# Kernel tuning notes

Measured on AMD Instinct MI355X. Metric: run time of the kernel, lower is better.

The kernel has to match this reference:

```python
import jax, jax.numpy as jnp
import numpy as np

NUM_TERMS = 8
NUM_CHANNELS = 64
BATCH = 8
NODES = 2048


def setup_inputs() -> dict:
    key = jax.random.key(0)
    kA, kh = jax.random.split(key)
    A = jax.random.normal(kA, (BATCH, NODES, NODES), dtype=jnp.float32)
    # xavier_uniform over (num_terms+1, num_channels)
    fan_in, fan_out = NUM_TERMS + 1, NUM_CHANNELS
    limit = float(np.sqrt(6.0 / (fan_in + fan_out)))
    h = jax.random.uniform(kh, (NUM_TERMS + 1, NUM_CHANNELS), dtype=jnp.float32,
                           minval=-limit, maxval=limit)
    return {"A": A, "h": h}


def reference(A, h):
    # Y[b,n,c] = h[0,c] + sum_{i=1..T} h[i,c] * diag(A^i)[b,n]
    num_terms = h.shape[0] - 1
    diags = []  # each [B, N]: diagonal of A^i
    Ap = A
    for i in range(num_terms):
        if i > 0:
            Ap = jnp.matmul(Ap, A)  # A^(i+1), computed once per power
        diags.append(jnp.diagonal(Ap, axis1=-2, axis2=-1))
    D = jnp.stack(diags, axis=0)  # [T, B, N]
    # fuse per-channel weighted sum of diagonals into one einsum
    out = jnp.einsum("tbn,tc->bnc", D, h[1:])
    out = out + h[0][None, None, :]  # identity term: diag(I) == 1
    return out
```

## Files before the change

kernel.cpp:

```cpp
#include <hip/hip_runtime.h>
#include <hip/hip_bf16.h>

#define NN 2048
#define BB 8
#define NC 64

typedef __bf16 bf16_8 __attribute__((ext_vector_type(8)));
typedef __bf16 bf16_4 __attribute__((ext_vector_type(4)));
typedef float f32x16 __attribute__((ext_vector_type(16)));

__device__ __forceinline__ void gll16(const void* g, void* l) {
  __builtin_amdgcn_global_load_lds((const __attribute__((address_space(1))) void*)g,
                                   (__attribute__((address_space(3))) void*)l,
                                   16, 0, 0);
}

__global__ __launch_bounds__(256)
void k_convert(const float* __restrict__ A, __bf16* __restrict__ Ab, __bf16* __restrict__ At) {
  __shared__ __bf16 tile[64][65];
  int b = blockIdx.z;
  const float* Asrc = A + (size_t)b * NN * NN;
  __bf16* Abd = Ab + (size_t)b * NN * NN;
  __bf16* Atd = At + (size_t)b * NN * NN;
  int r0 = blockIdx.y * 64, c0 = blockIdx.x * 64;
  int row = threadIdx.x >> 4;
  int col4 = (threadIdx.x & 15) * 4;
#pragma unroll
  for (int rr = 0; rr < 64; rr += 16) {
    float4 v = *(const float4*)&Asrc[(size_t)(r0 + row + rr) * NN + c0 + col4];
    bf16_4 hv;
    hv[0] = (__bf16)v.x; hv[1] = (__bf16)v.y; hv[2] = (__bf16)v.z; hv[3] = (__bf16)v.w;
    *(bf16_4*)&Abd[(size_t)(r0 + row + rr) * NN + c0 + col4] = hv;
    tile[row + rr][col4 + 0] = hv[0];
    tile[row + rr][col4 + 1] = hv[1];
    tile[row + rr][col4 + 2] = hv[2];
    tile[row + rr][col4 + 3] = hv[3];
  }
  __syncthreads();
  int row2 = threadIdx.x >> 3;
  int col8 = (threadIdx.x & 7) * 8;
#pragma unroll
  for (int rr = 0; rr < 64; rr += 32) {
    bf16_8 v;
#pragma unroll
    for (int j = 0; j < 8; ++j) v[j] = tile[col8 + j][row2 + rr];
    *(bf16_8*)&Atd[(size_t)(c0 + row2 + rr) * NN + r0 + col8] = v;
  }
}

__device__ __forceinline__
void gemm_body(const __bf16* __restrict__ Pb, const __bf16* __restrict__ Qb,
               __bf16* __restrict__ Cb, __bf16* __restrict__ Ctb,
               __bf16* smem, int tmBlk, int tnBlk) {
  __bf16 (*As)[64] = (__bf16(*)[64])smem;
  __bf16 (*Bs)[64] = (__bf16(*)[64])(smem + 16384);
  int tid = threadIdx.x;
  int wave = tid >> 6;
  int lane = tid & 63;
  int tm = tmBlk * 256;
  int tn = tnBlk * 128;
  int wm = (wave >> 1) * 128;
  int wn = (wave & 1) * 64;

  int srow = lane >> 3;
  int sc = (lane & 7) ^ srow;
  int arowA = wave * 64;
  int arowB = wave * 32;
  const __bf16* pA = Pb + (size_t)(tm + arowA + srow) * NN + sc * 8;
  const __bf16* pB = Qb + (size_t)(tn + arowB + srow) * NN + sc * 8;

  int am = lane & 31;
  int ah = lane >> 5;

  f32x16 acc[4][2] = {};

  for (int k0 = 0; k0 < NN; k0 += 64) {
#pragma unroll
    for (int g = 0; g < 8; ++g)
      gll16(pA + (size_t)(g * 8) * NN + k0, &As[arowA + g * 8][0]);
#pragma unroll
    for (int g = 0; g < 4; ++g)
      gll16(pB + (size_t)(g * 8) * NN + k0, &Bs[arowB + g * 8][0]);
    __syncthreads();
#pragma unroll
    for (int ks = 0; ks < 4; ++ks) {
      int cch = ks * 2 + ah;
      bf16_8 af[4], bf2[2];
#pragma unroll
      for (int i = 0; i < 4; ++i) {
        int ra = wm + i * 32 + am;
        af[i] = *(const bf16_8*)&As[ra][(cch ^ (ra & 7)) * 8];
      }
#pragma unroll
      for (int i = 0; i < 2; ++i) {
        int rb2 = wn + i * 32 + am;
        bf2[i] = *(const bf16_8*)&Bs[rb2][(cch ^ (rb2 & 7)) * 8];
      }
#pragma unroll
      for (int im = 0; im < 4; ++im)
#pragma unroll
        for (int in = 0; in < 2; ++in)
          acc[im][in] = __builtin_amdgcn_mfma_f32_32x32x16_bf16(af[im], bf2[in], acc[im][in], 0, 0, 0);
    }
    __syncthreads();
  }

  int cc = lane & 31;
  int rq = (lane >> 5) * 4;
#pragma unroll
  for (int im = 0; im < 4; ++im)
#pragma unroll
    for (int in = 0; in < 2; ++in)
#pragma unroll
      for (int reg = 0; reg < 16; ++reg) {
        int row = (reg & 3) + 8 * (reg >> 2) + rq;
        Cb[(size_t)(tm + wm + im * 32 + row) * NN + (tn + wn + in * 32 + cc)] =
            (__bf16)acc[im][in][reg];
      }

  if (Ctb != nullptr) {
    __bf16 (*Tt)[258] = (__bf16(*)[258])smem;
#pragma unroll
    for (int ch = 0; ch < 2; ++ch) {
      __syncthreads();
      if ((wave & 1) == ch) {
#pragma unroll
        for (int im = 0; im < 4; ++im)
#pragma unroll
          for (int in = 0; in < 2; ++in)
#pragma unroll
            for (int g = 0; g < 4; ++g) {
              bf16_4 v;
#pragma unroll
              for (int r = 0; r < 4; ++r) v[r] = (__bf16)acc[im][in][g * 4 + r];
              *(bf16_4*)&Tt[in * 32 + cc][wm + im * 32 + rq + 8 * g] = v;
            }
      }
      __syncthreads();
#pragma unroll
      for (int p = 0; p < 4; ++p) {
        int trow = p * 16 + (tid >> 4);
        int tcol = (tid & 15) * 16;
        bf16_8 v0 = *(const bf16_8*)&Tt[trow][tcol];
        bf16_8 v1 = *(const bf16_8*)&Tt[trow][tcol + 8];
        size_t gr = (size_t)(tn + ch * 64 + trow) * NN + tm + tcol;
        *(bf16_8*)&Ctb[gr] = v0;
        *(bf16_8*)&Ctb[gr + 8] = v1;
      }
    }
  }
}

__global__ __launch_bounds__(256, 2)
void k_gemm1(const __bf16* __restrict__ Ab, const __bf16* __restrict__ At,
             __bf16* __restrict__ A2, __bf16* __restrict__ A2t) {
  __shared__ __align__(16) __bf16 smem[24576];
  size_t mb = (size_t)blockIdx.z * NN * NN;
  gemm_body(Ab + mb, At + mb, A2 + mb, A2t + mb, smem, blockIdx.y, blockIdx.x);
}

__global__ __launch_bounds__(256, 3)
void k_gemm23(const __bf16* __restrict__ At, const __bf16* __restrict__ A2,
              const __bf16* __restrict__ A2t,
              __bf16* __restrict__ A3t, __bf16* __restrict__ A4,
              __bf16* __restrict__ A4t) {
  __shared__ __align__(16) __bf16 smem[24576];
  int job = blockIdx.z >> 3;
  size_t mb = (size_t)(blockIdx.z & 7) * NN * NN;
  if (job == 0)
    gemm_body(At + mb, A2 + mb, A3t + mb, nullptr, smem, blockIdx.y, blockIdx.x);
  else
    gemm_body(A2 + mb, A2t + mb, A4 + mb, A4t + mb, smem, blockIdx.y, blockIdx.x);
}

__global__ __launch_bounds__(256)
void k_reduce(const float* __restrict__ A, const float* __restrict__ h,
              const __bf16* __restrict__ A2, const __bf16* __restrict__ A3t,
              const __bf16* __restrict__ A4, const __bf16* __restrict__ A4t,
              float* __restrict__ out) {
  int b = blockIdx.y;
  int wave = threadIdx.x >> 6, lane = threadIdx.x & 63;
  int n = blockIdx.x * 4 + wave;
  size_t mb = (size_t)b * NN * NN;
  size_t rb = mb + (size_t)n * NN;
  float d5 = 0, d6 = 0, d7 = 0, d8 = 0;
  for (int c = 0; c < NN; c += 512) {
    int k = c + lane * 8;
    bf16_8 va2  = *(const bf16_8*)(A2 + rb + k);
    bf16_8 va3t = *(const bf16_8*)(A3t + rb + k);
    bf16_8 va4  = *(const bf16_8*)(A4 + rb + k);
    bf16_8 va4t = *(const bf16_8*)(A4t + rb + k);
#pragma unroll
    for (int j = 0; j < 8; ++j) {
      float f2 = (float)va2[j], f4 = (float)va4[j];
      float f3t = (float)va3t[j], f4t = (float)va4t[j];
      d5 += f2 * f3t;
      d6 += f2 * f4t;
      d7 += f4 * f3t;
      d8 += f4 * f4t;
    }
  }
#pragma unroll
  for (int off = 32; off > 0; off >>= 1) {
    d5 += __shfl_xor(d5, off);
    d6 += __shfl_xor(d6, off);
    d7 += __shfl_xor(d7, off);
    d8 += __shfl_xor(d8, off);
  }
  float d1 = A[mb + (size_t)n * NN + n];
  float d2 = (float)A2[rb + n];
  float d3 = (float)A3t[rb + n];
  float d4 = (float)A4[rb + n];
  float r = h[lane] + h[64 + lane] * d1 + h[128 + lane] * d2 + h[192 + lane] * d3 +
            h[256 + lane] * d4 + h[320 + lane] * d5 + h[384 + lane] * d6 +
            h[448 + lane] * d7 + h[512 + lane] * d8;
  out[((size_t)b * NN + n) * NC + lane] = r;
}

extern "C" void kernel_launch(void* const* d_in, const int* in_sizes, int n_in,
                              void* d_out, int out_size, void* d_ws, size_t ws_size,
                              hipStream_t stream) {
  const float* A = (const float*)d_in[0];
  const float* h = (const float*)d_in[1];
  float* out = (float*)d_out;

  size_t elems = (size_t)BB * NN * NN;
  __bf16* Ab  = (__bf16*)d_ws;
  __bf16* At  = Ab + elems;
  __bf16* A2  = At + elems;
  __bf16* A2t = A2 + elems;
  __bf16* A3t = A2t + elems;
  __bf16* A4  = A3t + elems;
  __bf16* A4t = Ab;

  dim3 bl(256);
  k_convert<<<dim3(32, 32, BB), bl, 0, stream>>>(A, Ab, At);
  k_gemm1<<<dim3(16, 8, BB), bl, 0, stream>>>(Ab, At, A2, A2t);
  k_gemm23<<<dim3(16, 8, 2 * BB), bl, 0, stream>>>(At, A2, A2t, A3t, A4, A4t);
  k_reduce<<<dim3(NN / 4, BB), bl, 0, stream>>>(A, h, A2, A3t, A4, A4t, out);
}
```

Before: 691.3 us.

## Rewrite GEMM as 256x256 tile, 8-wave kernel with double-buffered async LDS pipeline

Replaces the 256x128 tile GEMM, which had a single LDS buffer and barriers around every k-step, with a 256x256 tile on 512 threads (8 waves). A and B k-tiles are double-buffered in 128 KB of LDS. Global-to-LDS loads for later tiles are spread across eight phases and interleaved with MFMA work, using explicit vmcnt/lgkmcnt waits, s_barrier and s_setprio. The goal is to hide global memory latency and raise arithmetic intensity per block, at the cost of larger LDS use, fewer blocks, and fragile hand-placed synchronisation. The transposed-output epilogue is reworked to match the new wave layout.

```diff
diff --git a/kernel.cpp b/kernel.cpp
--- a/kernel.cpp
+++ b/kernel.cpp
@@ -4,6 +4,8 @@
 #define NN 2048
 #define BB 8
 #define NC 64
+#define NTILE 32
+#define NITER 16
 
 typedef __bf16 bf16_8 __attribute__((ext_vector_type(8)));
 typedef __bf16 bf16_4 __attribute__((ext_vector_type(4)));
@@ -49,64 +51,110 @@
 }
 
 __device__ __forceinline__
-void gemm_body(const __bf16* __restrict__ Pb, const __bf16* __restrict__ Qb,
-               __bf16* __restrict__ Cb, __bf16* __restrict__ Ctb,
-               __bf16* smem, int tmBlk, int tnBlk) {
-  __bf16 (*As)[64] = (__bf16(*)[64])smem;
-  __bf16 (*Bs)[64] = (__bf16(*)[64])(smem + 16384);
-  int tid = threadIdx.x;
-  int wave = tid >> 6;
-  int lane = tid & 63;
-  int tm = tmBlk * 256;
-  int tn = tnBlk * 128;
-  int wm = (wave >> 1) * 128;
-  int wn = (wave & 1) * 64;
-
-  int srow = lane >> 3;
-  int sc = (lane & 7) ^ srow;
-  int arowA = wave * 64;
-  int arowB = wave * 32;
-  const __bf16* pA = Pb + (size_t)(tm + arowA + srow) * NN + sc * 8;
-  const __bf16* pB = Qb + (size_t)(tn + arowB + srow) * NN + sc * 8;
-
-  int am = lane & 31;
-  int ah = lane >> 5;
+void gemm_body256(const __bf16* __restrict__ Pb, const __bf16* __restrict__ Qb,
+                  __bf16* __restrict__ Cb, __bf16* __restrict__ Ctb,
+                  __bf16* smem, int tmBlk, int tnBlk) {
+  __bf16 (*As)[256][64] = (__bf16(*)[256][64])smem;
+  __bf16 (*Bs)[256][64] = (__bf16(*)[256][64])(smem + 32768);
+  const int tid = threadIdx.x;
+  const int wave = tid >> 6, lane = tid & 63;
+  const int wm = wave >> 2, wn = wave & 3;
+  const int tm = tmBlk * 256, tn = tnBlk * 256;
+  const int am = lane & 31, ah = lane >> 5, rx = am & 7;
+
+  const int sr = lane >> 3;
+  const int sc = (lane & 7) ^ sr;
+  const __bf16* srcA = Pb + (size_t)(tm + wave * 8 + sr) * NN + sc * 8;
+  const __bf16* srcB = Qb + (size_t)(tn + wave * 8 + sr) * NN + sc * 8;
+
+#define STAGE(Tc_, s_, bufT_)                                                  \
+  do {                                                                         \
+    if ((s_) == 0) {                                                 \
+      const __bf16* s0 = srcA + (size_t)(Tc_) * 64;                            \
+      gll16(s0,                   &As[bufT_][wave * 8][0]);                    \
+      gll16(s0 + (size_t)64 * NN, &As[bufT_][64 + wave * 8][0]);               \
+    } else if ((s_) == 1) {                                          \
+      const __bf16* s0 = srcB + (size_t)128 * NN + (size_t)(Tc_) * 64;         \
+      gll16(s0,                   &Bs[bufT_][128 + wave * 8][0]);              \
+      gll16(s0 + (size_t)64 * NN, &Bs[bufT_][192 + wave * 8][0]);              \
+    } else if ((s_) == 2) {                                          \
+      const __bf16* s0 = srcA + (size_t)128 * NN + (size_t)(Tc_) * 64;         \
+      gll16(s0,                   &As[bufT_][128 + wave * 8][0]);              \
+      gll16(s0 + (size_t)64 * NN, &As[bufT_][192 + wave * 8][0]);              \
+    } else {                                                         \
+      const __bf16* s0 = srcB + (size_t)(Tc_) * 64;                            \
+      gll16(s0,                   &Bs[bufT_][wave * 8][0]);                    \
+      gll16(s0 + (size_t)64 * NN, &Bs[bufT_][64 + wave * 8][0]);               \
+    }                                                                          \
+  } while (0)
+
+  STAGE(0, 0, 0); STAGE(0, 3, 0); STAGE(0, 2, 0); STAGE(0, 1, 0);
+  STAGE(1, 0, 1); STAGE(1, 2, 1); STAGE(1, 1, 1);
+  asm volatile("s_waitcnt vmcnt(6)" ::: "memory");
+  __builtin_amdgcn_s_barrier();
 
   f32x16 acc[4][2] = {};
-
-  for (int k0 = 0; k0 < NN; k0 += 64) {
-#pragma unroll
-    for (int g = 0; g < 8; ++g)
-      gll16(pA + (size_t)(g * 8) * NN + k0, &As[arowA + g * 8][0]);
-#pragma unroll
-    for (int g = 0; g < 4; ++g)
-      gll16(pB + (size_t)(g * 8) * NN + k0, &Bs[arowB + g * 8][0]);
-    __syncthreads();
-#pragma unroll
-    for (int ks = 0; ks < 4; ++ks) {
-      int cch = ks * 2 + ah;
-      bf16_8 af[4], bf2[2];
-#pragma unroll
-      for (int i = 0; i < 4; ++i) {
-        int ra = wm + i * 32 + am;
-        af[i] = *(const bf16_8*)&As[ra][(cch ^ (ra & 7)) * 8];
-      }
-#pragma unroll
-      for (int i = 0; i < 2; ++i) {
-        int rb2 = wn + i * 32 + am;
-        bf2[i] = *(const bf16_8*)&Bs[rb2][(cch ^ (rb2 & 7)) * 8];
-      }
-#pragma unroll
-      for (int im = 0; im < 4; ++im)
-#pragma unroll
-        for (int in = 0; in < 2; ++in)
-          acc[im][in] = __builtin_amdgcn_mfma_f32_32x32x16_bf16(af[im], bf2[in], acc[im][in], 0, 0, 0);
+  bf16_8 af[2][4];
+
+  for (int it = 0; it < NITER; ++it) {
+#pragma unroll
+    for (int p = 0; p < 8; ++p) {
+      const int q = p & 3;
+      const int rbuf = p >> 2;
+      const int i0 = (q >> 1) * 2;
+      const int in = (q == 1 || q == 2) ? 1 : 0;
+      if ((q & 1) == 0) {
+#pragma unroll
+        for (int i = 0; i < 2; ++i) {
+          const int ra = (2 * (i0 + i) + wm) * 32 + am;
+#pragma unroll
+          for (int ks = 0; ks < 4; ++ks)
+            af[i][ks] = *(const bf16_8*)&As[rbuf][ra][((2 * ks + ah) ^ rx) * 8];
+        }
+      }
+      bf16_8 bfr[4];
+      {
+        const int rb = (in * 4 + wn) * 32 + am;
+#pragma unroll
+        for (int ks = 0; ks < 4; ++ks)
+          bfr[ks] = *(const bf16_8*)&Bs[rbuf][rb][((2 * ks + ah) ^ rx) * 8];
+      }
+      if (p == 0) {
+        int T = 2 * it + 1; STAGE(T, 3, 1);
+      } else if (p == 1) {
+        int T = 2 * it + 2; if (T > NTILE - 1) T = NTILE - 1;
+        STAGE(T, 0, 0);
+      } else if (p == 3) {
+        int T = 2 * it + 2; if (T > NTILE - 1) T = NTILE - 1;
+        STAGE(T, 2, 0); STAGE(T, 1, 0);
+      } else if (p == 4) {
+        int T = 2 * it + 2; if (T > NTILE - 1) T = NTILE - 1;
+        STAGE(T, 3, 0);
+      } else if (p == 5) {
+        int T = 2 * it + 3; if (T > NTILE - 1) T = NTILE - 1;
+        STAGE(T, 0, 1);
+      } else if (p == 7) {
+        int T = 2 * it + 3; if (T > NTILE - 1) T = NTILE - 1;
+        STAGE(T, 2, 1); STAGE(T, 1, 1);
+      }
+      __builtin_amdgcn_s_barrier();
+      asm volatile("s_waitcnt lgkmcnt(0)" ::: "memory");
+      __builtin_amdgcn_s_setprio(1);
+#pragma unroll
+      for (int ks = 0; ks < 4; ++ks)
+#pragma unroll
+        for (int i = 0; i < 2; ++i)
+          acc[i0 + i][in] = __builtin_amdgcn_mfma_f32_32x32x16_bf16(
+              af[i][ks], bfr[ks], acc[i0 + i][in], 0, 0, 0);
+      __builtin_amdgcn_s_setprio(0);
+      if (q == 3) asm volatile("s_waitcnt vmcnt(6)" ::: "memory");
+      __builtin_amdgcn_s_barrier();
     }
-    __syncthreads();
-  }
-
-  int cc = lane & 31;
-  int rq = (lane >> 5) * 4;
+  }
+  asm volatile("s_waitcnt vmcnt(0)" ::: "memory");
+
+  const int cc = am;
+  const int rq = ah * 4;
 #pragma unroll
   for (int im = 0; im < 4; ++im)
 #pragma unroll
@@ -114,63 +162,61 @@
 #pragma unroll
       for (int reg = 0; reg < 16; ++reg) {
         int row = (reg & 3) + 8 * (reg >> 2) + rq;
-        Cb[(size_t)(tm + wm + im * 32 + row) * NN + (tn + wn + in * 32 + cc)] =
-            (__bf16)acc[im][in][reg];
+        Cb[(size_t)(tm + (2 * im + wm) * 32 + row) * NN +
+           (tn + (4 * in + wn) * 32 + cc)] = (__bf16)acc[im][in][reg];
       }
 
   if (Ctb != nullptr) {
-    __bf16 (*Tt)[258] = (__bf16(*)[258])smem;
-#pragma unroll
-    for (int ch = 0; ch < 2; ++ch) {
+    __syncthreads();
+    __bf16 (*Tt)[264] = (__bf16(*)[264])smem;
+#pragma unroll
+    for (int ch = 0; ch < 4; ++ch) {
+      if ((wn >> 1) == (ch & 1)) {
+        const int inw = ch >> 1;
+#pragma unroll
+        for (int im = 0; im < 4; ++im)
+#pragma unroll
+          for (int g = 0; g < 4; ++g) {
+            bf16_4 v;
+#pragma unroll
+            for (int r = 0; r < 4; ++r) v[r] = (__bf16)acc[im][inw][g * 4 + r];
+            *(bf16_4*)&Tt[(wn & 1) * 32 + cc][(2 * im + wm) * 32 + 8 * g + rq] = v;
+          }
+      }
       __syncthreads();
-      if ((wave & 1) == ch) {
-#pragma unroll
-        for (int im = 0; im < 4; ++im)
-#pragma unroll
-          for (int in = 0; in < 2; ++in)
-#pragma unroll
-            for (int g = 0; g < 4; ++g) {
-              bf16_4 v;
-#pragma unroll
-              for (int r = 0; r < 4; ++r) v[r] = (__bf16)acc[im][in][g * 4 + r];
-              *(bf16_4*)&Tt[in * 32 + cc][wm + im * 32 + rq + 8 * g] = v;
-            }
+#pragma unroll
+      for (int rr = 0; rr < 4; ++rr) {
+        int trow = rr * 16 + (tid >> 5);
+        int tcol = (tid & 31) * 8;
+        bf16_8 v = *(const bf16_8*)&Tt[trow][tcol];
+        *(bf16_8*)&Ctb[(size_t)(tn + ch * 64 + trow) * NN + tm + tcol] = v;
       }
       __syncthreads();
-#pragma unroll
-      for (int p = 0; p < 4; ++p) {
-        int trow = p * 16 + (tid >> 4);
-        int tcol = (tid & 15) * 16;
-        bf16_8 v0 = *(const bf16_8*)&Tt[trow][tcol];
-        bf16_8 v1 = *(const bf16_8*)&Tt[trow][tcol + 8];
-        size_t gr = (size_t)(tn + ch * 64 + trow) * NN + tm + tcol;
-        *(bf16_8*)&Ctb[gr] = v0;
-        *(bf16_8*)&Ctb[gr + 8] = v1;
-      }
     }
   }
-}
-
-__global__ __launch_bounds__(256, 2)
+#undef STAGE
+}
+
+__global__ __launch_bounds__(512, 2)
 void k_gemm1(const __bf16* __restrict__ Ab, const __bf16* __restrict__ At,
              __bf16* __restrict__ A2, __bf16* __restrict__ A2t) {
-  __shared__ __align__(16) __bf16 smem[24576];
+  __shared__ __align__(16) __bf16 smem[65536];
   size_t mb = (size_t)blockIdx.z * NN * NN;
-  gemm_body(Ab + mb, At + mb, A2 + mb, A2t + mb, smem, blockIdx.y, blockIdx.x);
-}
-
-__global__ __launch_bounds__(256, 3)
+  gemm_body256(Ab + mb, At + mb, A2 + mb, A2t + mb, smem, blockIdx.y, blockIdx.x);
+}
+
+__global__ __launch_bounds__(512, 2)
 void k_gemm23(const __bf16* __restrict__ At, const __bf16* __restrict__ A2,
               const __bf16* __restrict__ A2t,
               __bf16* __restrict__ A3t, __bf16* __restrict__ A4,
               __bf16* __restrict__ A4t) {
-  __shared__ __align__(16) __bf16 smem[24576];
+  __shared__ __align__(16) __bf16 smem[65536];
   int job = blockIdx.z >> 3;
   size_t mb = (size_t)(blockIdx.z & 7) * NN * NN;
   if (job == 0)
-    gemm_body(At + mb, A2 + mb, A3t + mb, nullptr, smem, blockIdx.y, blockIdx.x);
+    gemm_body256(At + mb, A2 + mb, A3t + mb, nullptr, smem, blockIdx.y, blockIdx.x);
   else
-    gemm_body(A2 + mb, A2t + mb, A4 + mb, A4t + mb, smem, blockIdx.y, blockIdx.x);
+    gemm_body256(A2 + mb, A2t + mb, A4 + mb, A4t + mb, smem, blockIdx.y, blockIdx.x);
 }
 
 __global__ __launch_bounds__(256)
@@ -233,9 +279,8 @@
   __bf16* A4  = A3t + elems;
   __bf16* A4t = Ab;
 
-  dim3 bl(256);
-  k_convert<<<dim3(32, 32, BB), bl, 0, stream>>>(A, Ab, At);
-  k_gemm1<<<dim3(16, 8, BB), bl, 0, stream>>>(Ab, At, A2, A2t);
-  k_gemm23<<<dim3(16, 8, 2 * BB), bl, 0, stream>>>(At, A2, A2t, A3t, A4, A4t);
-  k_reduce<<<dim3(NN / 4, BB), bl, 0, stream>>>(A, h, A2, A3t, A4, A4t, out);
-}
+  k_convert<<<dim3(32, 32, BB), dim3(256), 0, stream>>>(A, Ab, At);
+  k_gemm1<<<dim3(8, 8, BB), dim3(512), 0, stream>>>(Ab, At, A2, A2t);
+  k_gemm23<<<dim3(8, 8, 2 * BB), dim3(512), 0, stream>>>(At, A2, A2t, A3t, A4, A4t);
+  k_reduce<<<dim3(NN / 4, BB), dim3(256), 0, stream>>>(A, h, A2, A3t, A4, A4t, out);
+}
```

Measured after the change: 696.9 us. No clear change (+0.8%).
